# Performance work log

Hardware: AMD Instinct MI355X
Metric: run time of the kernel (lower is better)

Reference implementation:

```python
import jax, jax.numpy as jnp
import numpy as np

B, H, W, C = 4, 64, 64, 32
M1 = M2 = 16
N = H * W          # 4096 grid nodes per sample
E = 131072         # edges (avg degree 32)
EDIM = 6           # edge feature dim
KMID = 64          # kernel MLP hidden width
EPS = 1e-5         # InstanceNorm eps


def _gelu(x):
    return jax.nn.gelu(x, approximate=False)  # torch nn.GELU default is exact erf


def _mlp(x, w1, b1, w2, b2):
    return _gelu(x @ w1 + b1) @ w2 + b2


def _inorm(x):
    # torch InstanceNorm2d(affine=False) applied to [B,H,W,C]: normalizes over last two dims
    m = x.mean(axis=(2, 3), keepdims=True)
    v = x.var(axis=(2, 3), keepdims=True)
    return (x - m) * jax.lax.rsqrt(v + EPS)


def _lin_init(k, fin, fout):
    lim = 1.0 / np.sqrt(fin)
    kw, kb = jax.random.split(k)
    w = jax.random.uniform(kw, (fin, fout), jnp.float32, -lim, lim)
    b = jax.random.uniform(kb, (fout,), jnp.float32, -lim, lim)
    return w, b


def setup_inputs() -> dict:
    key = jax.random.key(0)
    ks = jax.random.split(key, 14)
    s = 1.0 / (C * C)
    inp = {}
    inp['nodes'] = jax.random.normal(ks[0], (B, H, W, C), jnp.float32)
    inp['edge_index'] = jax.random.randint(ks[1], (2, E), 0, N, dtype=jnp.int64)
    inp['edge_attr'] = jax.random.uniform(ks[2], (E, EDIM), jnp.float32)
    # spectral conv complex weights, stored as real/imag float32 pairs
    inp['w1_re'] = s * jax.random.uniform(ks[3], (C, C, M1, M2), jnp.float32)
    inp['w1_im'] = s * jax.random.uniform(ks[4], (C, C, M1, M2), jnp.float32)
    inp['w2_re'] = s * jax.random.uniform(ks[5], (C, C, M1, M2), jnp.float32)
    inp['w2_im'] = s * jax.random.uniform(ks[6], (C, C, M1, M2), jnp.float32)
    # self.mlp : MLP(C, C, 2C)
    inp['mlp_w1'], inp['mlp_b1'] = _lin_init(ks[7], C, 2 * C)
    inp['mlp_w2'], inp['mlp_b2'] = _lin_init(ks[8], 2 * C, C)
    # self.w : MLP(C, C, 2C)
    inp['wm_w1'], inp['wm_b1'] = _lin_init(ks[9], C, 2 * C)
    inp['wm_w2'], inp['wm_b2'] = _lin_init(ks[10], 2 * C, C)
    # GNO kernel MLP : EDIM -> KMID -> C*C
    inp['ker_w1'], inp['ker_b1'] = _lin_init(ks[11], EDIM, KMID)
    inp['ker_w2'], inp['ker_b2'] = _lin_init(ks[12], KMID, C * C)
    # NNConv root weight and bias (PyG uniform(size) init with size=in_channels)
    lim = 1.0 / np.sqrt(C)
    kr, kb = jax.random.split(ks[13])
    inp['root'] = jax.random.uniform(kr, (C, C), jnp.float32, -lim, lim)
    inp['gbias'] = jax.random.uniform(kb, (C,), jnp.float32, -lim, lim)
    return inp


def reference(nodes, edge_index, edge_attr, w1_re, w1_im, w2_re, w2_im,
              mlp_w1, mlp_b1, mlp_w2, mlp_b2, wm_w1, wm_b1, wm_w2, wm_b2,
              ker_w1, ker_b1, ker_w2, ker_b2, root, gbias):
    x = _inorm(nodes)                                             # [B,H,W,C]

    # --- spectral conv branch ---
    x_ft = jnp.fft.rfftn(x, axes=(1, 2), norm='ortho')            # [B,H,W//2+1,C]
    w1 = (w1_re + 1j * w1_im).astype(jnp.complex64)
    w2 = (w2_re + 1j * w2_im).astype(jnp.complex64)
    top = jnp.einsum('bxyi,ioxy->bxyo', x_ft[:, :M1, :M2, :], w1)
    bot = jnp.einsum('bxyi,ioxy->bxyo', x_ft[:, -M1:, :M2, :], w2)
    out_ft = jnp.zeros((B, H, W // 2 + 1, C), jnp.complex64)
    out_ft = out_ft.at[:, :M1, :M2, :].set(top).at[:, -M1:, :M2, :].set(bot)
    x1 = jnp.fft.irfftn(out_ft, axes=(1, 2), s=(H, W), norm='ortho')
    x1 = _mlp(_inorm(x1), mlp_w1, mlp_b1, mlp_w2, mlp_b2)         # [B,H,W,C]

    # --- pointwise MLP branch ---
    x2 = _inorm(_mlp(x, wm_w1, wm_b1, wm_w2, wm_b2))              # [B,H,W,C]

    # --- edge-conditioned GNO branch ---
    x3 = x.reshape(B, N, C)
    wmat = _mlp(edge_attr, ker_w1, ker_b1, ker_w2, ker_b2).reshape(E, C, C)
    src, dst = edge_index[0], edge_index[1]
    msg = jnp.einsum('bec,eco->beo', x3[:, src, :], wmat)         # [B,E,C]
    agg = jnp.zeros((B, N, C), jnp.float32).at[:, dst, :].add(msg)
    x3 = agg + x3 @ root + gbias                                  # [B,N,C]

    return _gelu(x1 + x2 + x3.reshape(B, H, W, C))
```

## Files before the change

### kernel.cpp

```cpp
#include <hip/hip_runtime.h>

#define E_ 131072

typedef _Float16 half8 __attribute__((ext_vector_type(8)));
typedef float f32x4 __attribute__((ext_vector_type(4)));

__device__ __forceinline__ float gelu_f(float x) {
    return 0.5f * x * (1.0f + erff(x * 0.70710678118654752f));
}

#define TWOPI_64 (6.2831853071795864769f / 64.0f)

__device__ __forceinline__ void block_reduce2(float& s, float& s2, float* red) {
    #pragma unroll
    for (int off = 32; off > 0; off >>= 1) {
        s  += __shfl_down(s, off, 64);
        s2 += __shfl_down(s2, off, 64);
    }
    int lane = threadIdx.x & 63, wv = threadIdx.x >> 6;
    __syncthreads();
    if (lane == 0) { red[wv] = s; red[wv + 4] = s2; }
    __syncthreads();
    s  = red[0] + red[1] + red[2] + red[3];
    s2 = red[4] + red[5] + red[6] + red[7];
}

__device__ __forceinline__ void block_reduce2_w16(float& s, float& s2, float* red) {
    #pragma unroll
    for (int off = 32; off > 0; off >>= 1) {
        s  += __shfl_down(s, off, 64);
        s2 += __shfl_down(s2, off, 64);
    }
    int lane = threadIdx.x & 63, wv = threadIdx.x >> 6;
    __syncthreads();
    if (lane == 0) { red[wv] = s; red[wv + 16] = s2; }
    __syncthreads();
    float a = 0.f, b = 0.f;
    #pragma unroll
    for (int w = 0; w < 16; ++w) { a += red[w]; b += red[w + 16]; }
    s = a; s2 = b;
}

__device__ __forceinline__ void gno_body(int e0, float* sbufF, int* ssrc, int* sdst,
                                         const float* __restrict__ ea,
                                         const float* __restrict__ kw1, const float* __restrict__ kb1,
                                         const float* __restrict__ kb2,
                                         const _Float16* __restrict__ whi,
                                         const float* __restrict__ xn, const int* __restrict__ ei,
                                         float* __restrict__ agg) {
    _Float16* sxTh = (_Float16*)sbufF;
    int t = threadIdx.x;
    int lane = t & 63, wv = t >> 6, quad = lane >> 4, l15 = lane & 15;
    int eg = wv >> 1, t2 = wv & 1;

    if (t < 64) ssrc[t] = ei[e0 + t];
    else if (t < 128) sdst[t - 64] = ei[E_ + e0 + t - 64];
    {
        int r = t >> 2, k0 = (t & 3) * 16;
        const float* ep = ea + (e0 + r) * 6;
        float e6[6];
        #pragma unroll
        for (int d = 0; d < 6; ++d) e6[d] = ep[d];
        #pragma unroll
        for (int kk = 0; kk < 16; ++kk) {
            int k = k0 + kk;
            float acc = kb1[k];
            #pragma unroll
            for (int d = 0; d < 6; ++d) acc += e6[d] * kw1[d * 64 + k];
            sbufF[r * 68 + k] = gelu_f(acc);
        }
    }
    __syncthreads();
    half8 ahi[2][2], alo[2][2];
    #pragma unroll
    for (int et = 0; et < 2; ++et) {
        #pragma unroll
        for (int kh = 0; kh < 2; ++kh) {
            const float* hp = sbufF + (eg * 32 + et * 16 + l15) * 68 + kh * 32 + quad * 8;
            float4 h0 = *(const float4*)hp;
            float4 h1 = *(const float4*)(hp + 4);
            float hv[8] = {h0.x, h0.y, h0.z, h0.w, h1.x, h1.y, h1.z, h1.w};
            half8 hh, hl;
            #pragma unroll
            for (int j = 0; j < 8; ++j) {
                _Float16 hi = (_Float16)hv[j];
                hh[j] = hi;
                hl[j] = (_Float16)(hv[j] - (float)hi);
            }
            ahi[et][kh] = hh;
            alo[et][kh] = hl;
        }
    }
    __syncthreads();
    {
        int b = t & 3, r = t >> 2;
        int s = ssrc[r];
        int pe = (r >> 5) * 32 + ((r >> 2) & 3) * 8 + ((r >> 4) & 1) * 4 + (r & 3);
        const float4* xp = (const float4*)(xn + (b * 4096 + s) * 32);
        _Float16* dp = sxTh + b * 2312 + pe;
        #pragma unroll
        for (int q = 0; q < 8; ++q) {
            float4 v = xp[q];
            dp[(q * 4 + 0) * 72] = (_Float16)v.x;
            dp[(q * 4 + 1) * 72] = (_Float16)v.y;
            dp[(q * 4 + 2) * 72] = (_Float16)v.z;
            dp[(q * 4 + 3) * 72] = (_Float16)v.w;
        }
    }
    __syncthreads();
    float msg[4][2][4];
    #pragma unroll
    for (int b = 0; b < 4; ++b)
        #pragma unroll
        for (int et = 0; et < 2; ++et)
            #pragma unroll
            for (int r = 0; r < 4; ++r) msg[b][et][r] = 0.f;

    for (int i = 0; i < 32; ++i) {
        float b2v = kb2[i * 32 + t2 * 16 + l15];
        int f0 = (i * 4 + t2 * 2) * 512 + lane * 8;
        half8 bhi0 = *(const half8*)(whi + f0);
        half8 bhi1 = *(const half8*)(whi + f0 + 512);
        f32x4 acc[2];
        #pragma unroll
        for (int et = 0; et < 2; ++et) {
            f32x4 ac = {b2v, b2v, b2v, b2v};
            ac = __builtin_amdgcn_mfma_f32_16x16x32_f16(ahi[et][0], bhi0, ac, 0, 0, 0);
            ac = __builtin_amdgcn_mfma_f32_16x16x32_f16(ahi[et][1], bhi1, ac, 0, 0, 0);
            ac = __builtin_amdgcn_mfma_f32_16x16x32_f16(alo[et][0], bhi0, ac, 0, 0, 0);
            ac = __builtin_amdgcn_mfma_f32_16x16x32_f16(alo[et][1], bhi1, ac, 0, 0, 0);
            acc[et] = ac;
        }
        #pragma unroll
        for (int b = 0; b < 4; ++b) {
            const half8 xv = *(const half8*)(sxTh + b * 2312 + i * 72 + eg * 32 + quad * 8);
            #pragma unroll
            for (int et = 0; et < 2; ++et) {
                msg[b][et][0] += (float)xv[et * 4 + 0] * acc[et][0];
                msg[b][et][1] += (float)xv[et * 4 + 1] * acc[et][1];
                msg[b][et][2] += (float)xv[et * 4 + 2] * acc[et][2];
                msg[b][et][3] += (float)xv[et * 4 + 3] * acc[et][3];
            }
        }
    }
    int o = t2 * 16 + l15;
    #pragma unroll
    for (int et = 0; et < 2; ++et) {
        #pragma unroll
        for (int r = 0; r < 4; ++r) {
            int row = eg * 32 + et * 16 + quad * 4 + r;
            int d = sdst[row];
            #pragma unroll
            for (int b = 0; b < 4; ++b) {
                atomicAdd(&agg[(b * 4096 + d) * 32 + o], msg[b][et][r]);
            }
        }
    }
}

__global__ __launch_bounds__(1024, 1) void k_pre(const float* __restrict__ nodes,
                                                 const float* __restrict__ w2,
                                                 float* __restrict__ xn,
                                                 float* __restrict__ agg,
                                                 float* __restrict__ Gre, float* __restrict__ Gim,
                                                 _Float16* __restrict__ whi) {
    int t = threadIdx.x;
    if (blockIdx.x >= 256) {
        int g0 = (blockIdx.x - 256) * 4096 + t;
        #pragma unroll
        for (int r = 0; r < 4; ++r) {
            int g = g0 + r * 1024;
            int j = g & 7, l = (g >> 3) & 63, fid = g >> 9;
            int i = fid >> 2, t2 = (fid >> 1) & 1, kh = fid & 1;
            int quad = l >> 4, l15 = l & 15;
            int k = kh * 32 + quad * 8 + j;
            int n = i * 32 + t2 * 16 + l15;
            whi[g] = (_Float16)w2[k * 1024 + n];
        }
        return;
    }
    int bh = blockIdx.x;
    __shared__ float sx[2048];
    __shared__ float tc[64], ts[64];
    __shared__ float red[32];
    __shared__ float pre_[1024], pim_[1024];
    const float2* src = (const float2*)(nodes + bh * 2048);
    if (t < 64) { float a = TWOPI_64 * t; tc[t] = cosf(a); ts[t] = sinf(a); }
    float2 v = src[t];
    float s  = v.x + v.y;
    float s2 = v.x * v.x + v.y * v.y;
    block_reduce2_w16(s, s2, red);
    float mean = s * (1.0f / 2048.0f);
    float var  = s2 * (1.0f / 2048.0f) - mean * mean;
    float sc = rsqrtf(var + 1e-5f);
    v.x = (v.x - mean) * sc;
    v.y = (v.y - mean) * sc;
    ((float2*)(xn + bh * 2048))[t] = v;
    float2 z = {0.f, 0.f};
    ((float2*)(agg + bh * 2048))[t] = z;
    sx[t * 2] = v.x;
    sx[t * 2 + 1] = v.y;
    __syncthreads();
    {
        int oi = t & 511, half = t >> 9;
        int ky = oi >> 5, i = oi & 31;
        float re = 0.f, im = 0.f;
        int w0 = half * 32;
        #pragma unroll 8
        for (int w = w0; w < w0 + 32; ++w) {
            float vv = sx[w * 32 + i];
            int m = (ky * w) & 63;
            re += vv * tc[m];
            im -= vv * ts[m];
        }
        pre_[t] = re;
        pim_[t] = im;
    }
    __syncthreads();
    if (t < 512) {
        Gre[bh * 512 + t] = pre_[t] + pre_[t + 512];
        Gim[bh * 512 + t] = pim_[t] + pim_[t + 512];
    }
}

__global__ __launch_bounds__(256, 4) void k_g1(
        const float* __restrict__ Gre, const float* __restrict__ Gim,
        const float* __restrict__ w1re, const float* __restrict__ w1im,
        const float* __restrict__ w2re, const float* __restrict__ w2im,
        float* __restrict__ Yr, float* __restrict__ Yi,
        const float* __restrict__ ww1, const float* __restrict__ wb1,
        const float* __restrict__ ww2, const float* __restrict__ wb2,
        float* __restrict__ osum,
        const float* __restrict__ ea,
        const float* __restrict__ kw1, const float* __restrict__ kb1,
        const float* __restrict__ kb2,
        const _Float16* __restrict__ whi,
        const float* __restrict__ xn,
        const int* __restrict__ ei,
        float* __restrict__ agg) {
    __shared__ __align__(16) float U[4624];
    __shared__ int ssrc[64], sdst[64];
    int t = threadIdx.x;

    if (blockIdx.x < 128) {
        float* tc  = U;
        float* ts  = U + 64;
        float* sXr = U + 128;
        float* sXi = U + 656;
        int bid = blockIdx.x;
        int b = bid >> 5, kxi = bid & 31;
        int kx = kxi + (kxi < 16 ? 0 : 32);
        int x = kxi & 15;
        const float* wre = (kxi < 16) ? w1re : w2re;
        const float* wim = (kxi < 16) ? w1im : w2im;
        if (t < 64) { float a = TWOPI_64 * t; tc[t] = cosf(a); ts[t] = sinf(a); }
        __syncthreads();
        #pragma unroll 1
        for (int rep = 0; rep < 2; ++rep) {
            int oi = rep * 256 + t;
            int ky = oi >> 5, i = oi & 31;
            float re = 0.f, im = 0.f;
            #pragma unroll 8
            for (int h = 0; h < 64; ++h) {
                int gidx = (b * 64 + h) * 512 + ky * 32 + i;
                float gr = Gre[gidx], gi = Gim[gidx];
                int m = (kx * h) & 63;
                float c = tc[m], sv = ts[m];
                re += gr * c + gi * sv;
                im += gi * c - gr * sv;
            }
            sXr[ky * 33 + i] = re;
            sXi[ky * 33 + i] = im;
        }
        __syncthreads();
        #pragma unroll 1
        for (int rep = 0; rep < 2; ++rep) {
            int oi = rep * 256 + t;
            int ky = oi & 15, o = oi >> 4;
            float re = 0.f, im = 0.f;
            #pragma unroll 4
            for (int i = 0; i < 32; ++i) {
                float xr = sXr[ky * 33 + i], xi = sXi[ky * 33 + i];
                int widx = (i * 32 + o) * 256 + x * 16 + ky;
                float wr = wre[widx], wi = wim[widx];
                re += xr * wr - xi * wi;
                im += xr * wi + xi * wr;
            }
            Yr[bid * 512 + ky * 32 + o] = re;
            Yi[bid * 512 + ky * 32 + o] = im;
        }
        return;
    }
    if (blockIdx.x < 384) {
        int bh = blockIdx.x - 128;
        float* red = U;
        float* sX = U + 8;
        _Float16* sHh = (_Float16*)(U + 2120);
        for (int f = t; f < 2048; f += 256) sX[(f >> 5) * 33 + (f & 31)] = xn[bh * 2048 + f];
        __syncthreads();
        #pragma unroll 1
        for (int rep = 0; rep < 16; ++rep) {
            int idx = rep * 256 + t;
            int w = idx >> 6, k = idx & 63;
            float acc = wb1[k];
            #pragma unroll 4
            for (int c = 0; c < 32; ++c) acc += sX[w * 33 + c] * ww1[c * 64 + k];
            sHh[w * 72 + k] = (_Float16)gelu_f(acc);
        }
        __syncthreads();
        float s = 0.f, s2 = 0.f;
        #pragma unroll 1
        for (int rep = 0; rep < 8; ++rep) {
            int idx = rep * 256 + t;
            int w = idx >> 5, o = idx & 31;
            float acc = wb2[o];
            #pragma unroll 4
            for (int k = 0; k < 64; ++k) acc += (float)sHh[w * 72 + k] * ww2[k * 32 + o];
            sX[w * 33 + o] = acc;
            s += acc; s2 += acc * acc;
        }
        block_reduce2(s, s2, red);
        float mean = s * (1.0f / 2048.0f);
        float sc = rsqrtf(s2 * (1.0f / 2048.0f) - mean * mean + 1e-5f);
        #pragma unroll 1
        for (int rep = 0; rep < 8; ++rep) {
            int idx = rep * 256 + t;
            int w = idx >> 5, o = idx & 31;
            osum[bh * 2048 + idx] = (sX[w * 33 + o] - mean) * sc;
        }
        return;
    }
    gno_body((blockIdx.x - 384) * 64, U, ssrc, sdst,
             ea, kw1, kb1, kb2, whi, xn, ei, agg);
}

__global__ __launch_bounds__(1024, 1) void k_g2f(
        const float* __restrict__ Yr, const float* __restrict__ Yi,
        const float* __restrict__ mw1, const float* __restrict__ mb1,
        const float* __restrict__ mw2, const float* __restrict__ mb2,
        const float* __restrict__ osum, const float* __restrict__ agg,
        const float* __restrict__ xn, const float* __restrict__ root,
        const float* __restrict__ gbias, float* __restrict__ out) {
    __shared__ __align__(16) float U[8768];
    int t = threadIdx.x;
    int bh = blockIdx.x;
    int b = bh >> 6, h = bh & 63;
    float* tc  = U;
    float* ts  = U + 64;
    float* red = U + 128;
    float* sZr = U + 160;
    float* sZi = U + 688;
    float* sP  = U + 1216;
    _Float16* sHh = (_Float16*)(U + 3328);
    float* sX  = U + 5632;
    float* sR  = U + 7744;

    for (int f = t; f < 2048; f += 1024) sX[(f >> 5) * 33 + (f & 31)] = xn[bh * 2048 + f];
    if (t < 1024) { int f = t; sR[f] = root[f]; }
    float osv[2], agv[2];
    #pragma unroll
    for (int rep = 0; rep < 2; ++rep) {
        int idx = rep * 1024 + t;
        osv[rep] = osum[bh * 2048 + idx];
        agv[rep] = agg[bh * 2048 + idx];
    }
    if (t < 64) { float a = TWOPI_64 * t; tc[t] = cosf(a); ts[t] = sinf(a); }
    __syncthreads();
    if (t < 512) {
        int oi = t;
        int ky = oi >> 5, o = oi & 31;
        float re = 0.f, im = 0.f;
        #pragma unroll 4
        for (int kxi = 0; kxi < 32; ++kxi) {
            int kx = kxi + (kxi < 16 ? 0 : 32);
            int m = (kx * h) & 63;
            float c = tc[m], sv = ts[m];
            int yidx = (b * 32 + kxi) * 512 + ky * 32 + o;
            float yr = Yr[yidx], yi = Yi[yidx];
            re += yr * c - yi * sv;
            im += yr * sv + yi * c;
        }
        sZr[ky * 33 + o] = re;
        sZi[ky * 33 + o] = im;
    }
    __syncthreads();
    float s = 0.f, s2 = 0.f;
    #pragma unroll 1
    for (int rep = 0; rep < 2; ++rep) {
        int idx = rep * 1024 + t;
        int w = idx >> 5, o = idx & 31;
        float acc = sZr[o];
        #pragma unroll
        for (int ky = 1; ky < 16; ++ky) {
            int m = (ky * w) & 63;
            acc += 2.0f * (sZr[ky * 33 + o] * tc[m] - sZi[ky * 33 + o] * ts[m]);
        }
        acc *= (1.0f / 4096.0f);
        sP[w * 33 + o] = acc;
        s += acc; s2 += acc * acc;
    }
    block_reduce2_w16(s, s2, red);
    float mean = s * (1.0f / 2048.0f);
    float sc = rsqrtf(s2 * (1.0f / 2048.0f) - mean * mean + 1e-5f);
    #pragma unroll 1
    for (int rep = 0; rep < 2; ++rep) {
        int idx = rep * 1024 + t;
        int w = idx >> 5, o = idx & 31;
        sP[w * 33 + o] = (sP[w * 33 + o] - mean) * sc;
    }
    __syncthreads();
    #pragma unroll 1
    for (int rep = 0; rep < 4; ++rep) {
        int idx = rep * 1024 + t;
        int w = idx >> 6, k = idx & 63;
        float acc = mb1[k];
        #pragma unroll 4
        for (int c = 0; c < 32; ++c) acc += sP[w * 33 + c] * mw1[c * 64 + k];
        sHh[w * 72 + k] = (_Float16)gelu_f(acc);
    }
    __syncthreads();
    #pragma unroll 1
    for (int rep = 0; rep < 2; ++rep) {
        int idx = rep * 1024 + t;
        int w = idx >> 5, o = idx & 31;
        float x1v = mb2[o];
        #pragma unroll 4
        for (int k = 0; k < 64; ++k) x1v += (float)sHh[w * 72 + k] * mw2[k * 32 + o];
        float val = gbias[o] + osv[rep] + agv[rep] + x1v;
        #pragma unroll 4
        for (int c = 0; c < 32; ++c) val += sX[w * 33 + c] * sR[c * 32 + o];
        out[bh * 2048 + idx] = gelu_f(val);
    }
}

extern "C" void kernel_launch(void* const* d_in, const int* in_sizes, int n_in,
                              void* d_out, int out_size, void* d_ws, size_t ws_size,
                              hipStream_t stream) {
    (void)in_sizes; (void)n_in; (void)out_size; (void)ws_size;
    const float* nodes  = (const float*)d_in[0];
    const int*   eidx   = (const int*)d_in[1];
    const float* eattr  = (const float*)d_in[2];
    const float* w1re   = (const float*)d_in[3];
    const float* w1im   = (const float*)d_in[4];
    const float* w2re   = (const float*)d_in[5];
    const float* w2im   = (const float*)d_in[6];
    const float* mlp_w1 = (const float*)d_in[7];
    const float* mlp_b1 = (const float*)d_in[8];
    const float* mlp_w2 = (const float*)d_in[9];
    const float* mlp_b2 = (const float*)d_in[10];
    const float* wm_w1  = (const float*)d_in[11];
    const float* wm_b1  = (const float*)d_in[12];
    const float* wm_w2  = (const float*)d_in[13];
    const float* wm_b2  = (const float*)d_in[14];
    const float* ker_w1 = (const float*)d_in[15];
    const float* ker_b1 = (const float*)d_in[16];
    const float* ker_w2 = (const float*)d_in[17];
    const float* ker_b2 = (const float*)d_in[18];
    const float* root   = (const float*)d_in[19];
    const float* gbias  = (const float*)d_in[20];
    float* out = (float*)d_out;

    char* ws = (char*)d_ws;
    size_t off = 0;
    auto alloc = [&](size_t bytes) {
        void* p = ws + off;
        off += (bytes + 255) & ~(size_t)255;
        return p;
    };
    float* xn   = (float*)alloc(524288 * 4);
    float* agg  = (float*)alloc(524288 * 4);
    float* osum = (float*)alloc(524288 * 4);
    float* Gre  = (float*)alloc(131072 * 4);
    float* Gim  = (float*)alloc(131072 * 4);
    float* Yr   = (float*)alloc(65536 * 4);
    float* Yi   = (float*)alloc(65536 * 4);
    _Float16* whi = (_Float16*)alloc(65536 * 2);

    k_pre<<<272, 1024, 0, stream>>>(nodes, ker_w2, xn, agg, Gre, Gim, whi);
    k_g1<<<2432, 256, 0, stream>>>(Gre, Gim, w1re, w1im, w2re, w2im, Yr, Yi,
                                   wm_w1, wm_b1, wm_w2, wm_b2, osum,
                                   eattr, ker_w1, ker_b1, ker_b2, whi, xn, eidx, agg);
    k_g2f<<<256, 1024, 0, stream>>>(Yr, Yi, mlp_w1, mlp_b1, mlp_w2, mlp_b2,
                                    osum, agg, xn, root, gbias, out);
}
```

Baseline: 222.0 us.

## Merge spectral, pointwise and GNO stages into one persistent cooperative kernel

Replaces the k_g1 and k_g2f launches with a single cooperative persistent kernel that runs three phases separated by grid.sync. Phase one runs the spectral forward transform, the pointwise MLP and most GNO edge chunks. Phase two runs the inverse transform and the mlp branch, accumulating into osum while the remaining edge chunks run, and phase three applies the root matmul and final GELU. The goal is to remove a kernel launch boundary, overlap GNO work with the spectral tail, and drop the 1024-thread final kernel. In exchange it adds grid-wide barriers, occupancy-dependent scheduling and a read-modify-write of osum.

Result: slower. 872.7 us (+293.1%).

```diff
diff --git a/kernel.cpp b/kernel.cpp
--- a/kernel.cpp
+++ b/kernel.cpp
@@ -1,4 +1,7 @@
 #include <hip/hip_runtime.h>
+#include <hip/hip_cooperative_groups.h>
+
+namespace cg = cooperative_groups;
 
 #define E_ 131072
 
@@ -223,13 +226,15 @@
     }
 }
 
-__global__ __launch_bounds__(256, 4) void k_g1(
+__global__ __launch_bounds__(256, 7) void k_main(
         const float* __restrict__ Gre, const float* __restrict__ Gim,
         const float* __restrict__ w1re, const float* __restrict__ w1im,
         const float* __restrict__ w2re, const float* __restrict__ w2im,
         float* __restrict__ Yr, float* __restrict__ Yi,
         const float* __restrict__ ww1, const float* __restrict__ wb1,
         const float* __restrict__ ww2, const float* __restrict__ wb2,
+        const float* __restrict__ mw1, const float* __restrict__ mb1,
+        const float* __restrict__ mw2, const float* __restrict__ mb2,
         float* __restrict__ osum,
         const float* __restrict__ ea,
         const float* __restrict__ kw1, const float* __restrict__ kb1,
@@ -237,75 +242,143 @@
         const _Float16* __restrict__ whi,
         const float* __restrict__ xn,
         const int* __restrict__ ei,
-        float* __restrict__ agg) {
+        float* __restrict__ agg,
+        const float* __restrict__ root, const float* __restrict__ gbias,
+        float* __restrict__ out,
+        int G) {
     __shared__ __align__(16) float U[4624];
     __shared__ int ssrc[64], sdst[64];
     int t = threadIdx.x;
-
-    if (blockIdx.x < 128) {
-        float* tc  = U;
-        float* ts  = U + 64;
-        float* sXr = U + 128;
-        float* sXi = U + 656;
-        int bid = blockIdx.x;
-        int b = bid >> 5, kxi = bid & 31;
-        int kx = kxi + (kxi < 16 ? 0 : 32);
-        int x = kxi & 15;
-        const float* wre = (kxi < 16) ? w1re : w2re;
-        const float* wim = (kxi < 16) ? w1im : w2im;
+    int bid = blockIdx.x;
+    cg::grid_group grid = cg::this_grid();
+
+    for (int pt = bid; pt < 384; pt += G) {
+        __syncthreads();
+        if (pt < 128) {
+            float* tc  = U;
+            float* ts  = U + 64;
+            float* sXr = U + 128;
+            float* sXi = U + 656;
+            int b = pt >> 5, kxi = pt & 31;
+            int kx = kxi + (kxi < 16 ? 0 : 32);
+            int x = kxi & 15;
+            const float* wre = (kxi < 16) ? w1re : w2re;
+            const float* wim = (kxi < 16) ? w1im : w2im;
+            if (t < 64) { float a = TWOPI_64 * t; tc[t] = cosf(a); ts[t] = sinf(a); }
+            __syncthreads();
+            #pragma unroll 1
+            for (int rep = 0; rep < 2; ++rep) {
+                int oi = rep * 256 + t;
+                int ky = oi >> 5, i = oi & 31;
+                float re = 0.f, im = 0.f;
+                #pragma unroll 8
+                for (int h = 0; h < 64; ++h) {
+                    int gidx = (b * 64 + h) * 512 + ky * 32 + i;
+                    float gr = Gre[gidx], gi = Gim[gidx];
+                    int m = (kx * h) & 63;
+                    float c = tc[m], sv = ts[m];
+                    re += gr * c + gi * sv;
+                    im += gi * c - gr * sv;
+                }
+                sXr[ky * 33 + i] = re;
+                sXi[ky * 33 + i] = im;
+            }
+            __syncthreads();
+            #pragma unroll 1
+            for (int rep = 0; rep < 2; ++rep) {
+                int oi = rep * 256 + t;
+                int ky = oi & 15, o = oi >> 4;
+                float re = 0.f, im = 0.f;
+                #pragma unroll 4
+                for (int i = 0; i < 32; ++i) {
+                    float xr = sXr[ky * 33 + i], xi = sXi[ky * 33 + i];
+                    int widx = (i * 32 + o) * 256 + x * 16 + ky;
+                    float wr = wre[widx], wi = wim[widx];
+                    re += xr * wr - xi * wi;
+                    im += xr * wi + xi * wr;
+                }
+                Yr[pt * 512 + ky * 32 + o] = re;
+                Yi[pt * 512 + ky * 32 + o] = im;
+            }
+        } else {
+            int bh = pt - 128;
+            float* red = U;
+            float* sX = U + 8;
+            _Float16* sHh = (_Float16*)(U + 2120);
+            for (int f = t; f < 2048; f += 256) sX[(f >> 5) * 33 + (f & 31)] = xn[bh * 2048 + f];
+            __syncthreads();
+            #pragma unroll 1
+            for (int rep = 0; rep < 16; ++rep) {
+                int idx = rep * 256 + t;
+                int w = idx >> 6, k = idx & 63;
+                float acc = wb1[k];
+                #pragma unroll 4
+                for (int c = 0; c < 32; ++c) acc += sX[w * 33 + c] * ww1[c * 64 + k];
+                sHh[w * 72 + k] = (_Float16)gelu_f(acc);
+            }
+            __syncthreads();
+            float s = 0.f, s2 = 0.f;
+            #pragma unroll 1
+            for (int rep = 0; rep < 8; ++rep) {
+                int idx = rep * 256 + t;
+                int w = idx >> 5, o = idx & 31;
+                float acc = wb2[o];
+                #pragma unroll 4
+                for (int k = 0; k < 64; ++k) acc += (float)sHh[w * 72 + k] * ww2[k * 32 + o];
+                sX[w * 33 + o] = acc;
+                s += acc; s2 += acc * acc;
+            }
+            block_reduce2(s, s2, red);
+            float mean = s * (1.0f / 2048.0f);
+            float sc = rsqrtf(s2 * (1.0f / 2048.0f) - mean * mean + 1e-5f);
+            #pragma unroll 1
+            for (int rep = 0; rep < 8; ++rep) {
+                int idx = rep * 256 + t;
+                int w = idx >> 5, o = idx & 31;
+                osum[bh * 2048 + idx] = (sX[w * 33 + o] - mean) * sc;
+            }
+        }
+    }
+    {
+        int str1 = (G > 384) ? (G - 384) : 1;
+        for (int c = bid - 384; c >= 0 && c < 1536; c += str1) {
+            __syncthreads();
+            gno_body(c * 64, U, ssrc, sdst, ea, kw1, kb1, kb2, whi, xn, ei, agg);
+        }
+    }
+    __threadfence();
+    grid.sync();
+
+    for (int r = bid; r < 256; r += G) {
+        __syncthreads();
+        int bh = r;
+        int b = bh >> 6, h = bh & 63;
+        float* red = U;
+        float* sP  = U + 8;
+        float* sZr = U + 2120;
+        float* sZi = U + 2648;
+        float* tc  = U + 3176;
+        float* ts  = U + 3240;
+        _Float16* sHh = (_Float16*)(U + 2120);
         if (t < 64) { float a = TWOPI_64 * t; tc[t] = cosf(a); ts[t] = sinf(a); }
         __syncthreads();
         #pragma unroll 1
         for (int rep = 0; rep < 2; ++rep) {
             int oi = rep * 256 + t;
-            int ky = oi >> 5, i = oi & 31;
+            int ky = oi >> 5, o = oi & 31;
             float re = 0.f, im = 0.f;
-            #pragma unroll 8
-            for (int h = 0; h < 64; ++h) {
-                int gidx = (b * 64 + h) * 512 + ky * 32 + i;
-                float gr = Gre[gidx], gi = Gim[gidx];
+            #pragma unroll 4
+            for (int kxi = 0; kxi < 32; ++kxi) {
+                int kx = kxi + (kxi < 16 ? 0 : 32);
                 int m = (kx * h) & 63;
                 float c = tc[m], sv = ts[m];
-                re += gr * c + gi * sv;
-                im += gi * c - gr * sv;
-            }
-            sXr[ky * 33 + i] = re;
-            sXi[ky * 33 + i] = im;
-        }
-        __syncthreads();
-        #pragma unroll 1
-        for (int rep = 0; rep < 2; ++rep) {
-            int oi = rep * 256 + t;
-            int ky = oi & 15, o = oi >> 4;
-            float re = 0.f, im = 0.f;
-            #pragma unroll 4
-            for (int i = 0; i < 32; ++i) {
-                float xr = sXr[ky * 33 + i], xi = sXi[ky * 33 + i];
-                int widx = (i * 32 + o) * 256 + x * 16 + ky;
-                float wr = wre[widx], wi = wim[widx];
-                re += xr * wr - xi * wi;
-                im += xr * wi + xi * wr;
-            }
-            Yr[bid * 512 + ky * 32 + o] = re;
-            Yi[bid * 512 + ky * 32 + o] = im;
-        }
-        return;
-    }
-    if (blockIdx.x < 384) {
-        int bh = blockIdx.x - 128;
-        float* red = U;
-        float* sX = U + 8;
-        _Float16* sHh = (_Float16*)(U + 2120);
-        for (int f = t; f < 2048; f += 256) sX[(f >> 5) * 33 + (f & 31)] = xn[bh * 2048 + f];
-        __syncthreads();
-        #pragma unroll 1
-        for (int rep = 0; rep < 16; ++rep) {
-            int idx = rep * 256 + t;
-            int w = idx >> 6, k = idx & 63;
-            float acc = wb1[k];
-            #pragma unroll 4
-            for (int c = 0; c < 32; ++c) acc += sX[w * 33 + c] * ww1[c * 64 + k];
-            sHh[w * 72 + k] = (_Float16)gelu_f(acc);
+                int yidx = (b * 32 + kxi) * 512 + ky * 32 + o;
+                float yr = Yr[yidx], yi = Yi[yidx];
+                re += yr * c - yi * sv;
+                im += yr * sv + yi * c;
+            }
+            sZr[ky * 33 + o] = re;
+            sZi[ky * 33 + o] = im;
         }
         __syncthreads();
         float s = 0.f, s2 = 0.f;
@@ -313,10 +386,14 @@
         for (int rep = 0; rep < 8; ++rep) {
             int idx = rep * 256 + t;
             int w = idx >> 5, o = idx & 31;
-            float acc = wb2[o];
-            #pragma unroll 4
-            for (int k = 0; k < 64; ++k) acc += (float)sHh[w * 72 + k] * ww2[k * 32 + o];
-            sX[w * 33 + o] = acc;
+            float acc = sZr[o];
+            #pragma unroll
+            for (int ky = 1; ky < 16; ++ky) {
+                int m = (ky * w) & 63;
+                acc += 2.0f * (sZr[ky * 33 + o] * tc[m] - sZi[ky * 33 + o] * ts[m]);
+            }
+            acc *= (1.0f / 4096.0f);
+            sP[w * 33 + o] = acc;
             s += acc; s2 += acc * acc;
         }
         block_reduce2(s, s2, red);
@@ -326,110 +403,52 @@
         for (int rep = 0; rep < 8; ++rep) {
             int idx = rep * 256 + t;
             int w = idx >> 5, o = idx & 31;
-            osum[bh * 2048 + idx] = (sX[w * 33 + o] - mean) * sc;
-        }
-        return;
-    }
-    gno_body((blockIdx.x - 384) * 64, U, ssrc, sdst,
-             ea, kw1, kb1, kb2, whi, xn, ei, agg);
-}
-
-__global__ __launch_bounds__(1024, 1) void k_g2f(
-        const float* __restrict__ Yr, const float* __restrict__ Yi,
-        const float* __restrict__ mw1, const float* __restrict__ mb1,
-        const float* __restrict__ mw2, const float* __restrict__ mb2,
-        const float* __restrict__ osum, const float* __restrict__ agg,
-        const float* __restrict__ xn, const float* __restrict__ root,
-        const float* __restrict__ gbias, float* __restrict__ out) {
-    __shared__ __align__(16) float U[8768];
-    int t = threadIdx.x;
-    int bh = blockIdx.x;
-    int b = bh >> 6, h = bh & 63;
-    float* tc  = U;
-    float* ts  = U + 64;
-    float* red = U + 128;
-    float* sZr = U + 160;
-    float* sZi = U + 688;
-    float* sP  = U + 1216;
-    _Float16* sHh = (_Float16*)(U + 3328);
-    float* sX  = U + 5632;
-    float* sR  = U + 7744;
-
-    for (int f = t; f < 2048; f += 1024) sX[(f >> 5) * 33 + (f & 31)] = xn[bh * 2048 + f];
-    if (t < 1024) { int f = t; sR[f] = root[f]; }
-    float osv[2], agv[2];
-    #pragma unroll
-    for (int rep = 0; rep < 2; ++rep) {
-        int idx = rep * 1024 + t;
-        osv[rep] = osum[bh * 2048 + idx];
-        agv[rep] = agg[bh * 2048 + idx];
-    }
-    if (t < 64) { float a = TWOPI_64 * t; tc[t] = cosf(a); ts[t] = sinf(a); }
-    __syncthreads();
-    if (t < 512) {
-        int oi = t;
-        int ky = oi >> 5, o = oi & 31;
-        float re = 0.f, im = 0.f;
+            sP[w * 33 + o] = (sP[w * 33 + o] - mean) * sc;
+        }
+        __syncthreads();
+        #pragma unroll 1
+        for (int rep = 0; rep < 16; ++rep) {
+            int idx = rep * 256 + t;
+            int w = idx >> 6, k = idx & 63;
+            float acc = mb1[k];
+            #pragma unroll 4
+            for (int c = 0; c < 32; ++c) acc += sP[w * 33 + c] * mw1[c * 64 + k];
+            sHh[w * 72 + k] = (_Float16)gelu_f(acc);
+        }
+        __syncthreads();
+        #pragma unroll 1
+        for (int rep = 0; rep < 8; ++rep) {
+            int idx = rep * 256 + t;
+            int w = idx >> 5, o = idx & 31;
+            float acc = mb2[o];
+            #pragma unroll 4
+            for (int k = 0; k < 64; ++k) acc += (float)sHh[w * 72 + k] * mw2[k * 32 + o];
+            osum[bh * 2048 + idx] += acc;
+        }
+    }
+    {
+        int str2 = (G > 256) ? (G - 256) : 1;
+        for (int c = bid - 256; c >= 0 && c < 512; c += str2) {
+            __syncthreads();
+            gno_body((1536 + c) * 64, U, ssrc, sdst, ea, kw1, kb1, kb2, whi, xn, ei, agg);
+        }
+    }
+    __threadfence();
+    grid.sync();
+
+    for (int task = bid; task < 2048; task += G) {
+        __syncthreads();
+        int base = task * 256;
+        float* sX = U;
+        float* sR = U + 264;
+        sX[(t >> 5) * 33 + (t & 31)] = xn[base + t];
+        for (int f = t; f < 1024; f += 256) sR[f] = root[f];
+        __syncthreads();
+        int w = t >> 5, o = t & 31;
+        float acc = gbias[o] + osum[base + t] + agg[base + t];
         #pragma unroll 4
-        for (int kxi = 0; kxi < 32; ++kxi) {
-            int kx = kxi + (kxi < 16 ? 0 : 32);
-            int m = (kx * h) & 63;
-            float c = tc[m], sv = ts[m];
-            int yidx = (b * 32 + kxi) * 512 + ky * 32 + o;
-            float yr = Yr[yidx], yi = Yi[yidx];
-            re += yr * c - yi * sv;
-            im += yr * sv + yi * c;
-        }
-        sZr[ky * 33 + o] = re;
-        sZi[ky * 33 + o] = im;
-    }
-    __syncthreads();
-    float s = 0.f, s2 = 0.f;
-    #pragma unroll 1
-    for (int rep = 0; rep < 2; ++rep) {
-        int idx = rep * 1024 + t;
-        int w = idx >> 5, o = idx & 31;
-        float acc = sZr[o];
-        #pragma unroll
-        for (int ky = 1; ky < 16; ++ky) {
-            int m = (ky * w) & 63;
-            acc += 2.0f * (sZr[ky * 33 + o] * tc[m] - sZi[ky * 33 + o] * ts[m]);
-        }
-        acc *= (1.0f / 4096.0f);
-        sP[w * 33 + o] = acc;
-        s += acc; s2 += acc * acc;
-    }
-    block_reduce2_w16(s, s2, red);
-    float mean = s * (1.0f / 2048.0f);
-    float sc = rsqrtf(s2 * (1.0f / 2048.0f) - mean * mean + 1e-5f);
-    #pragma unroll 1
-    for (int rep = 0; rep < 2; ++rep) {
-        int idx = rep * 1024 + t;
-        int w = idx >> 5, o = idx & 31;
-        sP[w * 33 + o] = (sP[w * 33 + o] - mean) * sc;
-    }
-    __syncthreads();
-    #pragma unroll 1
-    for (int rep = 0; rep < 4; ++rep) {
-        int idx = rep * 1024 + t;
-        int w = idx >> 6, k = idx & 63;
-        float acc = mb1[k];
-        #pragma unroll 4
-        for (int c = 0; c < 32; ++c) acc += sP[w * 33 + c] * mw1[c * 64 + k];
-        sHh[w * 72 + k] = (_Float16)gelu_f(acc);
-    }
-    __syncthreads();
-    #pragma unroll 1
-    for (int rep = 0; rep < 2; ++rep) {
-        int idx = rep * 1024 + t;
-        int w = idx >> 5, o = idx & 31;
-        float x1v = mb2[o];
-        #pragma unroll 4
-        for (int k = 0; k < 64; ++k) x1v += (float)sHh[w * 72 + k] * mw2[k * 32 + o];
-        float val = gbias[o] + osv[rep] + agv[rep] + x1v;
-        #pragma unroll 4
-        for (int c = 0; c < 32; ++c) val += sX[w * 33 + c] * sR[c * 32 + o];
-        out[bh * 2048 + idx] = gelu_f(val);
+        for (int c = 0; c < 32; ++c) acc += sX[w * 33 + c] * sR[c * 32 + o];
+        out[base + t] = gelu_f(acc);
     }
 }
 
@@ -477,9 +496,29 @@
     _Float16* whi = (_Float16*)alloc(65536 * 2);
 
     k_pre<<<272, 1024, 0, stream>>>(nodes, ker_w2, xn, agg, Gre, Gim, whi);
-    k_g1<<<2432, 256, 0, stream>>>(Gre, Gim, w1re, w1im, w2re, w2im, Yr, Yi,
-                                   wm_w1, wm_b1, wm_w2, wm_b2, osum,
-                                   eattr, ker_w1, ker_b1, ker_b2, whi, xn, eidx, agg);
-    k_g2f<<<256, 1024, 0, stream>>>(Yr, Yi, mlp_w1, mlp_b1, mlp_w2, mlp_b2,
-                                    osum, agg, xn, root, gbias, out);
-}
+
+    int occ = 0;
+    hipOccupancyMaxActiveBlocksPerMultiprocessor(&occ, k_main, 256, 0);
+    if (occ < 1) occ = 1;
+    int G = occ * 256;
+    if (G > 2048) G = 2048;
+
+    void* args[] = {
+        (void*)&Gre, (void*)&Gim,
+        (void*)&w1re, (void*)&w1im, (void*)&w2re, (void*)&w2im,
+        (void*)&Yr, (void*)&Yi,
+        (void*)&wm_w1, (void*)&wm_b1, (void*)&wm_w2, (void*)&wm_b2,
+        (void*)&mlp_w1, (void*)&mlp_b1, (void*)&mlp_w2, (void*)&mlp_b2,
+        (void*)&osum,
+        (void*)&eattr,
+        (void*)&ker_w1, (void*)&ker_b1, (void*)&ker_b2,
+        (void*)&whi,
+        (void*)&xn,
+        (void*)&eidx,
+        (void*)&agg,
+        (void*)&root, (void*)&gbias,
+        (void*)&out,
+        (void*)&G
+    };
+    hipLaunchCooperativeKernel(k_main, dim3(G), dim3(256), args, 0, stream);
+}
```
